# Optimization experiments

Hardware: AMD Instinct MI355X
Metric: run time of the kernel (lower is better)

## Reference

```python
import jax, jax.numpy as jnp
import numpy as np

N_NODES = 20000
D = 256            # input_dim (forced by 32x16 reshape: 2*D == 512)
N_EDGES = 320000


def _init(key, shape, scale=0.02):
    return scale * jax.random.normal(key, shape, jnp.float32)


def setup_inputs() -> dict:
    key = jax.random.key(0)
    ks = jax.random.split(key, 20)
    x = jax.random.normal(ks[0], (N_NODES, D), jnp.float32)
    edge = jax.random.randint(ks[1], (N_EDGES, 2), 0, N_NODES, dtype=jnp.int64)
    params = dict(
        W_gcn=_init(ks[2], (D, 2 * D)), b_gcn=jnp.zeros((2 * D,), jnp.float32),
        conv1_w=_init(ks[3], (1, 1, 3, 3)), conv1_b=jnp.zeros((1,), jnp.float32),
        conv2_w=_init(ks[4], (1, 1, 3, 3)), conv2_b=jnp.zeros((1,), jnp.float32),
        Wc1=_init(ks[5], (2 * D, 2 * D)), bc1=jnp.zeros((2 * D,), jnp.float32),
        Wc2=_init(ks[6], (2 * D, 2 * D)), bc2=jnp.zeros((2 * D,), jnp.float32),
        Wc3=_init(ks[7], (2 * D, 2 * D)), bc3=jnp.zeros((2 * D,), jnp.float32),
        Wp1=_init(ks[8], (4 * D, 2 * D)), bp1=jnp.zeros((2 * D,), jnp.float32),
        Wp2=_init(ks[9], (2 * D, D)), bp2=jnp.zeros((D,), jnp.float32),
        Wp3=_init(ks[10], (D, D // 2)), bp3=jnp.zeros((D // 2,), jnp.float32),
        Wp4=_init(ks[11], (D // 2, 2)), bp4=jnp.zeros((2,), jnp.float32),
    )
    return dict(x=x, edge=edge, **params)


def _gcn_conv(x, edge, W, b):
    # PyG GCNConv: add self-loops, symmetric deg^-1/2 normalization, scatter-add at dst
    src, dst = edge[:, 0], edge[:, 1]
    loops = jnp.arange(N_NODES, dtype=edge.dtype)
    src = jnp.concatenate([src, loops])
    dst = jnp.concatenate([dst, loops])
    xw = x @ W                                              # [N, 2D]
    deg = jax.ops.segment_sum(jnp.ones_like(dst, jnp.float32), dst, N_NODES)
    dinv = jnp.where(deg > 0, jax.lax.rsqrt(jnp.maximum(deg, 1e-12)), 0.0)
    norm = dinv[src] * dinv[dst]                            # [E+N]
    agg = jax.ops.segment_sum(norm[:, None] * xw[src], dst, N_NODES)
    return agg + b


def reference(x, edge, W_gcn, b_gcn, conv1_w, conv1_b, conv2_w, conv2_b,
              Wc1, bc1, Wc2, bc2, Wc3, bc3,
              Wp1, bp1, Wp2, bp2, Wp3, bp3, Wp4, bp4):
    # First stage: GCNConv + ReLU, then sum readout over nodes -> [1, 2D]
    h = jax.nn.relu(_gcn_conv(x, edge, W_gcn, b_gcn))
    h = jnp.sum(h, axis=0, keepdims=True)                   # [1, 512]

    img = h.reshape(1, 1, 32, 16)
    dn = ('NCHW', 'OIHW', 'NCHW')
    c = jax.nn.relu(jax.lax.conv_general_dilated(img, conv1_w, (1, 1), 'SAME', dimension_numbers=dn) + conv1_b.reshape(1, -1, 1, 1))
    c = jax.nn.relu(jax.lax.conv_general_dilated(c, conv2_w, (1, 1), 'SAME', dimension_numbers=dn) + conv2_b.reshape(1, -1, 1, 1))
    high_conf = jax.nn.softmax(c.reshape(1, -1), axis=1)    # [1, 512]

    # Second stage, branch B: 3-layer MLP with softmax
    f = jax.nn.relu(h @ Wc1 + bc1)
    f = jax.nn.relu(f @ Wc2 + bc2)
    front = jax.nn.softmax(f @ Wc3 + bc3, axis=1)           # [1, 512]

    complete = jnp.concatenate([high_conf, front], axis=1)  # [1, 1024]

    # Predictor MLP: 1024 -> 512 -> 256 -> 128 -> 2, sigmoid
    p = jax.nn.relu(complete @ Wp1 + bp1)
    p = jax.nn.relu(p @ Wp2 + bp2)
    p = jax.nn.relu(p @ Wp3 + bp3)
    pre = jax.nn.sigmoid(p @ Wp4 + bp4)                     # [1, 2]
    return pre
```

## Files before the change

### kernel.cpp

```cpp
#include <hip/hip_runtime.h>

#define N_NODES 20000
#define N_EDGES 320000
#define DD      256
#define D2      512
#define BCAP    64

typedef short short8 __attribute__((ext_vector_type(8)));
typedef float f32x4  __attribute__((ext_vector_type(4)));
typedef float f32x2  __attribute__((ext_vector_type(2)));

__device__ __forceinline__ unsigned f2b(float f) {
    unsigned u = __float_as_uint(f);
    u = u + 0x7fffu + ((u >> 16) & 1u);
    return u >> 16;
}

__device__ __forceinline__ unsigned f2e4m3(float f) {
    unsigned u = __float_as_uint(f);
    unsigned sg = (u >> 24) & 0x80u;
    float af = fabsf(f);
    if (af > 448.f) return sg | 0x7Eu;
    if (af < 0.015625f) {
        int i = (int)rintf(af * 512.f);
        return sg | (unsigned)i;
    }
    unsigned au = u & 0x7fffffffu;
    au += 0x7ffffu + ((au >> 20) & 1u);
    unsigned b = (au >> 20) - 960u;
    if (b > 0x7Eu) b = 0x7Eu;
    return sg | b;
}

__global__ void k1_prep(const int* __restrict__ edge, int* __restrict__ cnt,
                        int* __restrict__ csr, const float* __restrict__ x,
                        const float* __restrict__ Wg, unsigned short* __restrict__ WT,
                        unsigned* __restrict__ xf8) {
    int blk = blockIdx.x, tid = threadIdx.x;
    if (blk < 1250) {
        int e = blk * 256 + tid;
        if (e < N_EDGES) {
            int s = edge[2 * e], d = edge[2 * e + 1];
            int pos = atomicAdd(&cnt[d], 1);
            if (pos < BCAP) csr[d * BCAP + pos] = s;
        }
    } else if (blk < 1282) {
        int i = (blk - 1250) * 256 + tid;
        #pragma unroll
        for (int r = 0; r < 16; r++) {
            int idx = i + r * 8192;
            int k = idx >> 9, n = idx & 511;
            WT[n * 256 + k] = (unsigned short)f2b(Wg[idx]);
        }
    } else {
        int i = (blk - 1282) * 256 + tid;
        float4 v = ((const float4*)x)[i];
        xf8[i] = f2e4m3(v.x) | (f2e4m3(v.y) << 8) | (f2e4m3(v.z) << 16) | (f2e4m3(v.w) << 24);
    }
}

__device__ __forceinline__ float dinv_of(const int* cnt, int n) {
    return rsqrtf((float)(cnt[n] + 1));
}
__device__ __forceinline__ void acc8(float* a, float w, uint2 u) {
    f32x2 p;
    p = __builtin_amdgcn_cvt_pk_f32_fp8(u.x, false); a[0] += w * p.x; a[1] += w * p.y;
    p = __builtin_amdgcn_cvt_pk_f32_fp8(u.x, true);  a[2] += w * p.x; a[3] += w * p.y;
    p = __builtin_amdgcn_cvt_pk_f32_fp8(u.y, false); a[4] += w * p.x; a[5] += w * p.y;
    p = __builtin_amdgcn_cvt_pk_f32_fp8(u.y, true);  a[6] += w * p.x; a[7] += w * p.y;
}

__global__ void k4_agg(const int* __restrict__ cnt, const int* __restrict__ csr,
                       const unsigned char* __restrict__ xf8,
                       unsigned short* __restrict__ aggX) {
    int wid = threadIdx.x >> 6, lane = threadIdx.x & 63;
    int half = lane >> 5, l32 = lane & 31;
    int n = blockIdx.x * 4 + wid;
    float a[8] = {0.f, 0.f, 0.f, 0.f, 0.f, 0.f, 0.f, 0.f};
    if (n < N_NODES) {
        int deg = cnt[n];
        if (deg > BCAP) deg = BCAP;
        const int* bkt = csr + n * BCAP;
        int e = 0;
        for (; e + 8 <= deg; e += 8) {
            int s0 = bkt[e + 0 + half];
            int s1 = bkt[e + 2 + half];
            int s2 = bkt[e + 4 + half];
            int s3 = bkt[e + 6 + half];
            uint2 u0 = *(const uint2*)(xf8 + (size_t)s0 * DD + l32 * 8);
            uint2 u1 = *(const uint2*)(xf8 + (size_t)s1 * DD + l32 * 8);
            uint2 u2 = *(const uint2*)(xf8 + (size_t)s2 * DD + l32 * 8);
            uint2 u3 = *(const uint2*)(xf8 + (size_t)s3 * DD + l32 * 8);
            float w0 = dinv_of(cnt, s0), w1 = dinv_of(cnt, s1);
            float w2 = dinv_of(cnt, s2), w3 = dinv_of(cnt, s3);
            acc8(a, w0, u0); acc8(a, w1, u1); acc8(a, w2, u2); acc8(a, w3, u3);
        }
        for (; e + 2 <= deg; e += 2) {
            int s = bkt[e + half];
            uint2 u = *(const uint2*)(xf8 + (size_t)s * DD + l32 * 8);
            acc8(a, dinv_of(cnt, s), u);
        }
        if (e < deg && half == 0) {
            int s = bkt[e];
            uint2 u = *(const uint2*)(xf8 + (size_t)s * DD + l32 * 8);
            acc8(a, dinv_of(cnt, s), u);
        }
        #pragma unroll
        for (int j = 0; j < 8; j++) a[j] += __shfl_xor(a[j], 32, 64);
        float dn = dinv_of(cnt, n);
        float dn2 = dn * dn;
        uint2 u = *(const uint2*)(xf8 + (size_t)n * DD + l32 * 8);
        f32x2 p;
        p = __builtin_amdgcn_cvt_pk_f32_fp8(u.x, false); a[0] = dn * a[0] + dn2 * p.x; a[1] = dn * a[1] + dn2 * p.y;
        p = __builtin_amdgcn_cvt_pk_f32_fp8(u.x, true);  a[2] = dn * a[2] + dn2 * p.x; a[3] = dn * a[3] + dn2 * p.y;
        p = __builtin_amdgcn_cvt_pk_f32_fp8(u.y, false); a[4] = dn * a[4] + dn2 * p.x; a[5] = dn * a[5] + dn2 * p.y;
        p = __builtin_amdgcn_cvt_pk_f32_fp8(u.y, true);  a[6] = dn * a[6] + dn2 * p.x; a[7] = dn * a[7] + dn2 * p.y;
    }
    if (half == 0) {
        uint4 o;
        o.x = f2b(a[0]) | (f2b(a[1]) << 16);
        o.y = f2b(a[2]) | (f2b(a[3]) << 16);
        o.z = f2b(a[4]) | (f2b(a[5]) << 16);
        o.w = f2b(a[6]) | (f2b(a[7]) << 16);
        *(uint4*)(aggX + (size_t)n * DD + l32 * 8) = o;
    }
}

#define TN 128
__global__ void __launch_bounds__(256, 2)
k5_gemm(const unsigned short* __restrict__ aggX, const unsigned short* __restrict__ WT,
        const float* __restrict__ bg, float* __restrict__ h) {
    __shared__ unsigned short bsh[TN * 264];
    __shared__ float hblk[TN];
    int tid = threadIdx.x;
    int rowblk = blockIdx.x;
    int ct = blockIdx.y;
    #pragma unroll
    for (int i = 0; i < 16; i++) {
        int c = tid + i * 256;
        int r = c >> 5;
        int kc = (c & 31) << 3;
        *(short8*)(&bsh[r * 264 + kc]) = *(const short8*)(WT + (size_t)(ct * TN + r) * DD + kc);
    }
    if (tid < TN) hblk[tid] = 0.f;
    __syncthreads();

    int w = tid >> 6, lane = tid & 63;
    int quad = lane >> 4, l15 = lane & 15;
    int row = rowblk * 64 + w * 16 + l15;
    f32x4 acc[8];
    #pragma unroll
    for (int nt = 0; nt < 8; nt++) acc[nt] = (f32x4){0.f, 0.f, 0.f, 0.f};
    #pragma unroll
    for (int kt = 0; kt < 8; kt++) {
        short8 a = *(const short8*)(aggX + (size_t)row * DD + kt * 32 + quad * 8);
        #pragma unroll
        for (int nt = 0; nt < 8; nt++) {
            short8 b = *(const short8*)(&bsh[(nt * 16 + l15) * 264 + kt * 32 + quad * 8]);
            acc[nt] = __builtin_amdgcn_mfma_f32_16x16x32_bf16(a, b, acc[nt], 0, 0, 0);
        }
    }
    int rowbase = rowblk * 64 + w * 16 + quad * 4;
    #pragma unroll
    for (int nt = 0; nt < 8; nt++) {
        int cl = nt * 16 + l15;
        float bias = bg[ct * TN + cl];
        float s = 0.f;
        #pragma unroll
        for (int r = 0; r < 4; r++) {
            if (rowbase + r < N_NODES) {
                float v = acc[nt][r] + bias;
                s += v > 0.f ? v : 0.f;
            }
        }
        atomicAdd(&hblk[cl], s);
    }
    __syncthreads();
    if (tid < TN) atomicAdd(&h[ct * TN + tid], hblk[tid]);
}

__global__ void k_mv(const float* __restrict__ in, const float* __restrict__ bias,
                     const float* __restrict__ W, float* __restrict__ out, int N, int act) {
    int c = blockIdx.y * 256 + threadIdx.x;
    int k0 = blockIdx.x * 8;
    float s = 0.f;
    #pragma unroll
    for (int kk = 0; kk < 8; kk++) {
        int k = k0 + kk;
        float v = in[k];
        if (act) { v += bias[k]; v = v > 0.f ? v : 0.f; }
        s += v * W[(size_t)k * N + c];
    }
    atomicAdd(&out[c], s);
}

__global__ void k9_mid(const float* __restrict__ h, const float* __restrict__ w1, const float* __restrict__ b1,
                       const float* __restrict__ w2, const float* __restrict__ b2,
                       const float* __restrict__ l3raw, const float* __restrict__ bc3,
                       float* __restrict__ complete) {
    __shared__ float img[512];
    __shared__ float c1s[512];
    __shared__ float red[512];
    int t = threadIdx.x;
    img[t] = h[t];
    __syncthreads();
    int y = t >> 4, x = t & 15;
    float s = 0.f;
    #pragma unroll
    for (int dy = -1; dy <= 1; dy++)
        #pragma unroll
        for (int dx = -1; dx <= 1; dx++) {
            int yy = y + dy, xc = x + dx;
            if (yy >= 0 && yy < 32 && xc >= 0 && xc < 16)
                s += w1[(dy + 1) * 3 + (dx + 1)] * img[yy * 16 + xc];
        }
    s += b1[0];
    c1s[t] = s > 0.f ? s : 0.f;
    __syncthreads();
    float s2 = 0.f;
    #pragma unroll
    for (int dy = -1; dy <= 1; dy++)
        #pragma unroll
        for (int dx = -1; dx <= 1; dx++) {
            int yy = y + dy, xc = x + dx;
            if (yy >= 0 && yy < 32 && xc >= 0 && xc < 16)
                s2 += w2[(dy + 1) * 3 + (dx + 1)] * c1s[yy * 16 + xc];
        }
    s2 += b2[0];
    float v2 = s2 > 0.f ? s2 : 0.f;
    red[t] = v2; __syncthreads();
    for (int off = 256; off > 0; off >>= 1) { if (t < off) red[t] = fmaxf(red[t], red[t + off]); __syncthreads(); }
    float m = red[0]; __syncthreads();
    float e = expf(v2 - m);
    red[t] = e; __syncthreads();
    for (int off = 256; off > 0; off >>= 1) { if (t < off) red[t] += red[t + off]; __syncthreads(); }
    complete[t] = e / red[0];
    __syncthreads();
    float z = l3raw[t] + bc3[t];
    red[t] = z; __syncthreads();
    for (int off = 256; off > 0; off >>= 1) { if (t < off) red[t] = fmaxf(red[t], red[t + off]); __syncthreads(); }
    float m2 = red[0]; __syncthreads();
    float e2 = expf(z - m2);
    red[t] = e2; __syncthreads();
    for (int off = 256; off > 0; off >>= 1) { if (t < off) red[t] += red[t + off]; __syncthreads(); }
    complete[512 + t] = e2 / red[0];
}

__global__ void k12_final(const float* __restrict__ p2raw, const float* __restrict__ bp2,
                          const float* __restrict__ Wp3, const float* __restrict__ bp3,
                          const float* __restrict__ Wp4, const float* __restrict__ bp4,
                          float* __restrict__ out) {
    __shared__ float p2s[256];
    __shared__ float p3s[128];
    int t = threadIdx.x;
    float v = p2raw[t] + bp2[t];
    p2s[t] = v > 0.f ? v : 0.f;
    __syncthreads();
    if (t < 128) {
        float s = bp3[t];
        #pragma unroll 8
        for (int k = 0; k < 256; k++) s += p2s[k] * Wp3[k * 128 + t];
        p3s[t] = s > 0.f ? s : 0.f;
    }
    __syncthreads();
    if (t < 2) {
        float s = bp4[t];
        for (int k = 0; k < 128; k++) s += p3s[k] * Wp4[k * 2 + t];
        out[t] = 1.f / (1.f + expf(-s));
    }
}

extern "C" void kernel_launch(void* const* d_in, const int* in_sizes, int n_in,
                              void* d_out, int out_size, void* d_ws, size_t ws_size,
                              hipStream_t stream) {
    const float* x    = (const float*)d_in[0];
    const int*   edge = (const int*)d_in[1];
    const float* Wg   = (const float*)d_in[2];
    const float* bg   = (const float*)d_in[3];
    const float* c1w  = (const float*)d_in[4];
    const float* c1b  = (const float*)d_in[5];
    const float* c2w  = (const float*)d_in[6];
    const float* c2b  = (const float*)d_in[7];
    const float* Wc1  = (const float*)d_in[8];
    const float* bc1  = (const float*)d_in[9];
    const float* Wc2  = (const float*)d_in[10];
    const float* bc2  = (const float*)d_in[11];
    const float* Wc3  = (const float*)d_in[12];
    const float* bc3  = (const float*)d_in[13];
    const float* Wp1  = (const float*)d_in[14];
    const float* bp1  = (const float*)d_in[15];
    const float* Wp2  = (const float*)d_in[16];
    const float* bp2  = (const float*)d_in[17];
    const float* Wp3  = (const float*)d_in[18];
    const float* bp3  = (const float*)d_in[19];
    const float* Wp4  = (const float*)d_in[20];
    const float* bp4  = (const float*)d_in[21];
    float* out = (float*)d_out;

    char* ws = (char*)d_ws;
    int*   cnt      = (int*)(ws + 0);
    float* h        = (float*)(ws + 80000);
    float* f1raw    = (float*)(ws + 82048);
    float* f2raw    = (float*)(ws + 84096);
    float* l3raw    = (float*)(ws + 86144);
    float* p1raw    = (float*)(ws + 88192);
    float* p2raw    = (float*)(ws + 90240);
    float* complete = (float*)(ws + 91264);
    int*   csr      = (int*)(ws + 95360);
    unsigned short* WT   = (unsigned short*)(ws + 5215360);
    unsigned char*  xf8  = (unsigned char*)(ws + 5477504);
    unsigned short* aggX = (unsigned short*)(ws + 10597504);
    (void)ws_size; (void)in_sizes; (void)n_in; (void)out_size;

    hipMemsetAsync(d_ws, 0, 91264, stream);

    k1_prep<<<6282, 256, 0, stream>>>(edge, cnt, csr, x, Wg, WT, (unsigned*)xf8);
    k4_agg<<<5008, 256, 0, stream>>>(cnt, csr, xf8, aggX);
    k5_gemm<<<dim3(313, 4), 256, 0, stream>>>(aggX, WT, bg, h);
    k_mv<<<dim3(64, 2), 256, 0, stream>>>(h,     nullptr, Wc1, f1raw, 512, 0);
    k_mv<<<dim3(64, 2), 256, 0, stream>>>(f1raw, bc1,     Wc2, f2raw, 512, 1);
    k_mv<<<dim3(64, 2), 256, 0, stream>>>(f2raw, bc2,     Wc3, l3raw, 512, 1);
    k9_mid<<<1, 512, 0, stream>>>(h, c1w, c1b, c2w, c2b, l3raw, bc3, complete);
    k_mv<<<dim3(128, 2), 256, 0, stream>>>(complete, nullptr, Wp1, p1raw, 512, 0);
    k_mv<<<dim3(64, 1), 256, 0, stream>>>(p1raw, bp1, Wp2, p2raw, 256, 1);
    k12_final<<<1, 256, 0, stream>>>(p2raw, bp2, Wp3, bp3, Wp4, bp4, out);
}
```

Before: 214.5 us.

## Fuse tail MLP kernels via last-block pattern, deepen aggregation unroll, reduce atomics

Merges the single-block conv/softmax kernel into the preceding matrix-vector kernel and the final predictor kernel into its matrix-vector kernel, using a done counter so the last block to finish runs the tail. This removes two kernel launches and their gaps. The aggregation loop is unrolled to 16 edges so more gathers are in flight, and the GEMM epilogue reduces across quads with shuffles before the shared-memory atomic. The tradeoffs are extra fences and counter atomics, the tail now running in a single 256-thread block, and higher register pressure in the aggregation loop.

```diff
diff --git a/kernel.cpp b/kernel.cpp
--- a/kernel.cpp
+++ b/kernel.cpp
@@ -30,6 +30,10 @@
     unsigned b = (au >> 20) - 960u;
     if (b > 0x7Eu) b = 0x7Eu;
     return sg | b;
+}
+
+__device__ __forceinline__ float aload(const float* p) {
+    return __hip_atomic_load(p, __ATOMIC_RELAXED, __HIP_MEMORY_SCOPE_AGENT);
 }
 
 __global__ void k1_prep(const int* __restrict__ edge, int* __restrict__ cnt,
@@ -82,18 +86,33 @@
         if (deg > BCAP) deg = BCAP;
         const int* bkt = csr + n * BCAP;
         int e = 0;
-        for (; e + 8 <= deg; e += 8) {
-            int s0 = bkt[e + 0 + half];
-            int s1 = bkt[e + 2 + half];
-            int s2 = bkt[e + 4 + half];
-            int s3 = bkt[e + 6 + half];
+        for (; e + 16 <= deg; e += 16) {
+            int s0 = bkt[e + 0 + half],  s1 = bkt[e + 2 + half];
+            int s2 = bkt[e + 4 + half],  s3 = bkt[e + 6 + half];
+            int s4 = bkt[e + 8 + half],  s5 = bkt[e + 10 + half];
+            int s6 = bkt[e + 12 + half], s7 = bkt[e + 14 + half];
             uint2 u0 = *(const uint2*)(xf8 + (size_t)s0 * DD + l32 * 8);
             uint2 u1 = *(const uint2*)(xf8 + (size_t)s1 * DD + l32 * 8);
             uint2 u2 = *(const uint2*)(xf8 + (size_t)s2 * DD + l32 * 8);
             uint2 u3 = *(const uint2*)(xf8 + (size_t)s3 * DD + l32 * 8);
-            float w0 = dinv_of(cnt, s0), w1 = dinv_of(cnt, s1);
-            float w2 = dinv_of(cnt, s2), w3 = dinv_of(cnt, s3);
-            acc8(a, w0, u0); acc8(a, w1, u1); acc8(a, w2, u2); acc8(a, w3, u3);
+            uint2 u4 = *(const uint2*)(xf8 + (size_t)s4 * DD + l32 * 8);
+            uint2 u5 = *(const uint2*)(xf8 + (size_t)s5 * DD + l32 * 8);
+            uint2 u6 = *(const uint2*)(xf8 + (size_t)s6 * DD + l32 * 8);
+            uint2 u7 = *(const uint2*)(xf8 + (size_t)s7 * DD + l32 * 8);
+            acc8(a, dinv_of(cnt, s0), u0); acc8(a, dinv_of(cnt, s1), u1);
+            acc8(a, dinv_of(cnt, s2), u2); acc8(a, dinv_of(cnt, s3), u3);
+            acc8(a, dinv_of(cnt, s4), u4); acc8(a, dinv_of(cnt, s5), u5);
+            acc8(a, dinv_of(cnt, s6), u6); acc8(a, dinv_of(cnt, s7), u7);
+        }
+        for (; e + 8 <= deg; e += 8) {
+            int s0 = bkt[e + 0 + half], s1 = bkt[e + 2 + half];
+            int s2 = bkt[e + 4 + half], s3 = bkt[e + 6 + half];
+            uint2 u0 = *(const uint2*)(xf8 + (size_t)s0 * DD + l32 * 8);
+            uint2 u1 = *(const uint2*)(xf8 + (size_t)s1 * DD + l32 * 8);
+            uint2 u2 = *(const uint2*)(xf8 + (size_t)s2 * DD + l32 * 8);
+            uint2 u3 = *(const uint2*)(xf8 + (size_t)s3 * DD + l32 * 8);
+            acc8(a, dinv_of(cnt, s0), u0); acc8(a, dinv_of(cnt, s1), u1);
+            acc8(a, dinv_of(cnt, s2), u2); acc8(a, dinv_of(cnt, s3), u3);
         }
         for (; e + 2 <= deg; e += 2) {
             int s = bkt[e + half];
@@ -173,7 +192,9 @@
                 s += v > 0.f ? v : 0.f;
             }
         }
-        atomicAdd(&hblk[cl], s);
+        s += __shfl_xor(s, 16, 64);
+        s += __shfl_xor(s, 32, 64);
+        if (quad == 0) atomicAdd(&hblk[cl], s);
     }
     __syncthreads();
     if (tid < TN) atomicAdd(&h[ct * TN + tid], hblk[tid]);
@@ -194,79 +215,136 @@
     atomicAdd(&out[c], s);
 }
 
-__global__ void k9_mid(const float* __restrict__ h, const float* __restrict__ w1, const float* __restrict__ b1,
-                       const float* __restrict__ w2, const float* __restrict__ b2,
-                       const float* __restrict__ l3raw, const float* __restrict__ bc3,
-                       float* __restrict__ complete) {
+__global__ void k_mv_k9(const float* __restrict__ in, const float* __restrict__ bias,
+                        const float* __restrict__ W, float* __restrict__ l3raw,
+                        const float* __restrict__ h,
+                        const float* __restrict__ c1w, const float* __restrict__ c1b,
+                        const float* __restrict__ c2w, const float* __restrict__ c2b,
+                        const float* __restrict__ bc3,
+                        float* __restrict__ complete, int* __restrict__ done) {
     __shared__ float img[512];
     __shared__ float c1s[512];
-    __shared__ float red[512];
-    int t = threadIdx.x;
-    img[t] = h[t];
-    __syncthreads();
-    int y = t >> 4, x = t & 15;
-    float s = 0.f;
-    #pragma unroll
-    for (int dy = -1; dy <= 1; dy++)
-        #pragma unroll
-        for (int dx = -1; dx <= 1; dx++) {
-            int yy = y + dy, xc = x + dx;
-            if (yy >= 0 && yy < 32 && xc >= 0 && xc < 16)
-                s += w1[(dy + 1) * 3 + (dx + 1)] * img[yy * 16 + xc];
-        }
-    s += b1[0];
-    c1s[t] = s > 0.f ? s : 0.f;
-    __syncthreads();
-    float s2 = 0.f;
-    #pragma unroll
-    for (int dy = -1; dy <= 1; dy++)
-        #pragma unroll
-        for (int dx = -1; dx <= 1; dx++) {
-            int yy = y + dy, xc = x + dx;
-            if (yy >= 0 && yy < 32 && xc >= 0 && xc < 16)
-                s2 += w2[(dy + 1) * 3 + (dx + 1)] * c1s[yy * 16 + xc];
-        }
-    s2 += b2[0];
-    float v2 = s2 > 0.f ? s2 : 0.f;
-    red[t] = v2; __syncthreads();
-    for (int off = 256; off > 0; off >>= 1) { if (t < off) red[t] = fmaxf(red[t], red[t + off]); __syncthreads(); }
+    __shared__ float red[256];
+    __shared__ int lastflag;
+    int tid = threadIdx.x;
+    {
+        int c = blockIdx.y * 256 + tid;
+        int k0 = blockIdx.x * 8;
+        float s = 0.f;
+        #pragma unroll
+        for (int kk = 0; kk < 8; kk++) {
+            int k = k0 + kk;
+            float v = in[k] + bias[k];
+            v = v > 0.f ? v : 0.f;
+            s += v * W[k * 512 + c];
+        }
+        atomicAdd(&l3raw[c], s);
+    }
+    __threadfence();
+    if (tid == 0) lastflag = (atomicAdd(done, 1) == 127);
+    __syncthreads();
+    if (!lastflag) return;
+    __threadfence();
+    img[tid] = h[tid]; img[tid + 256] = h[tid + 256];
+    __syncthreads();
+    float cv[2];
+    #pragma unroll
+    for (int p = 0; p < 2; p++) {
+        int pix = tid + p * 256;
+        int y = pix >> 4, x = pix & 15;
+        float s = 0.f;
+        #pragma unroll
+        for (int dy = -1; dy <= 1; dy++)
+            #pragma unroll
+            for (int dx = -1; dx <= 1; dx++) {
+                int yy = y + dy, xc = x + dx;
+                if (yy >= 0 && yy < 32 && xc >= 0 && xc < 16)
+                    s += c1w[(dy + 1) * 3 + (dx + 1)] * img[yy * 16 + xc];
+            }
+        s += c1b[0];
+        cv[p] = s > 0.f ? s : 0.f;
+    }
+    c1s[tid] = cv[0]; c1s[tid + 256] = cv[1];
+    __syncthreads();
+    float v2[2];
+    #pragma unroll
+    for (int p = 0; p < 2; p++) {
+        int pix = tid + p * 256;
+        int y = pix >> 4, x = pix & 15;
+        float s = 0.f;
+        #pragma unroll
+        for (int dy = -1; dy <= 1; dy++)
+            #pragma unroll
+            for (int dx = -1; dx <= 1; dx++) {
+                int yy = y + dy, xc = x + dx;
+                if (yy >= 0 && yy < 32 && xc >= 0 && xc < 16)
+                    s += c2w[(dy + 1) * 3 + (dx + 1)] * c1s[yy * 16 + xc];
+            }
+        s += c2b[0];
+        v2[p] = s > 0.f ? s : 0.f;
+    }
+    red[tid] = fmaxf(v2[0], v2[1]); __syncthreads();
+    for (int off = 128; off > 0; off >>= 1) { if (tid < off) red[tid] = fmaxf(red[tid], red[tid + off]); __syncthreads(); }
     float m = red[0]; __syncthreads();
-    float e = expf(v2 - m);
-    red[t] = e; __syncthreads();
-    for (int off = 256; off > 0; off >>= 1) { if (t < off) red[t] += red[t + off]; __syncthreads(); }
-    complete[t] = e / red[0];
-    __syncthreads();
-    float z = l3raw[t] + bc3[t];
-    red[t] = z; __syncthreads();
-    for (int off = 256; off > 0; off >>= 1) { if (t < off) red[t] = fmaxf(red[t], red[t + off]); __syncthreads(); }
+    float e0 = expf(v2[0] - m), e1 = expf(v2[1] - m);
+    red[tid] = e0 + e1; __syncthreads();
+    for (int off = 128; off > 0; off >>= 1) { if (tid < off) red[tid] += red[tid + off]; __syncthreads(); }
+    float inv = 1.f / red[0];
+    complete[tid] = e0 * inv; complete[tid + 256] = e1 * inv;
+    __syncthreads();
+    float z0 = aload(&l3raw[tid]) + bc3[tid];
+    float z1 = aload(&l3raw[tid + 256]) + bc3[tid + 256];
+    red[tid] = fmaxf(z0, z1); __syncthreads();
+    for (int off = 128; off > 0; off >>= 1) { if (tid < off) red[tid] = fmaxf(red[tid], red[tid + off]); __syncthreads(); }
     float m2 = red[0]; __syncthreads();
-    float e2 = expf(z - m2);
-    red[t] = e2; __syncthreads();
-    for (int off = 256; off > 0; off >>= 1) { if (t < off) red[t] += red[t + off]; __syncthreads(); }
-    complete[512 + t] = e2 / red[0];
-}
-
-__global__ void k12_final(const float* __restrict__ p2raw, const float* __restrict__ bp2,
-                          const float* __restrict__ Wp3, const float* __restrict__ bp3,
-                          const float* __restrict__ Wp4, const float* __restrict__ bp4,
-                          float* __restrict__ out) {
+    float g0 = expf(z0 - m2), g1 = expf(z1 - m2);
+    red[tid] = g0 + g1; __syncthreads();
+    for (int off = 128; off > 0; off >>= 1) { if (tid < off) red[tid] += red[tid + off]; __syncthreads(); }
+    float inv2 = 1.f / red[0];
+    complete[512 + tid] = g0 * inv2; complete[768 + tid] = g1 * inv2;
+}
+
+__global__ void k_mv_k12(const float* __restrict__ in, const float* __restrict__ bias,
+                         const float* __restrict__ W, float* __restrict__ p2raw,
+                         const float* __restrict__ bp2,
+                         const float* __restrict__ Wp3, const float* __restrict__ bp3,
+                         const float* __restrict__ Wp4, const float* __restrict__ bp4,
+                         float* __restrict__ out, int* __restrict__ done) {
     __shared__ float p2s[256];
     __shared__ float p3s[128];
-    int t = threadIdx.x;
-    float v = p2raw[t] + bp2[t];
-    p2s[t] = v > 0.f ? v : 0.f;
-    __syncthreads();
-    if (t < 128) {
-        float s = bp3[t];
+    __shared__ int lastflag;
+    int tid = threadIdx.x;
+    {
+        int k0 = blockIdx.x * 8;
+        float s = 0.f;
+        #pragma unroll
+        for (int kk = 0; kk < 8; kk++) {
+            int k = k0 + kk;
+            float v = in[k] + bias[k];
+            v = v > 0.f ? v : 0.f;
+            s += v * W[k * 256 + tid];
+        }
+        atomicAdd(&p2raw[tid], s);
+    }
+    __threadfence();
+    if (tid == 0) lastflag = (atomicAdd(done, 1) == 63);
+    __syncthreads();
+    if (!lastflag) return;
+    __threadfence();
+    float v = aload(&p2raw[tid]) + bp2[tid];
+    p2s[tid] = v > 0.f ? v : 0.f;
+    __syncthreads();
+    if (tid < 128) {
+        float s = bp3[tid];
         #pragma unroll 8
-        for (int k = 0; k < 256; k++) s += p2s[k] * Wp3[k * 128 + t];
-        p3s[t] = s > 0.f ? s : 0.f;
-    }
-    __syncthreads();
-    if (t < 2) {
-        float s = bp4[t];
-        for (int k = 0; k < 128; k++) s += p3s[k] * Wp4[k * 2 + t];
-        out[t] = 1.f / (1.f + expf(-s));
+        for (int k = 0; k < 256; k++) s += p2s[k] * Wp3[k * 128 + tid];
+        p3s[tid] = s > 0.f ? s : 0.f;
+    }
+    __syncthreads();
+    if (tid < 2) {
+        float s = bp4[tid];
+        for (int k = 0; k < 128; k++) s += p3s[k] * Wp4[k * 2 + tid];
+        out[tid] = 1.f / (1.f + expf(-s));
     }
 }
 
@@ -305,23 +383,25 @@
     float* l3raw    = (float*)(ws + 86144);
     float* p1raw    = (float*)(ws + 88192);
     float* p2raw    = (float*)(ws + 90240);
-    float* complete = (float*)(ws + 91264);
-    int*   csr      = (int*)(ws + 95360);
-    unsigned short* WT   = (unsigned short*)(ws + 5215360);
-    unsigned char*  xf8  = (unsigned char*)(ws + 5477504);
-    unsigned short* aggX = (unsigned short*)(ws + 10597504);
+    int*   done9    = (int*)(ws + 91264);
+    int*   done12   = (int*)(ws + 91268);
+    float* complete = (float*)(ws + 91280);
+    int*   csr      = (int*)(ws + 95376);
+    unsigned short* WT   = (unsigned short*)(ws + 5215376);
+    unsigned char*  xf8  = (unsigned char*)(ws + 5477520);
+    unsigned short* aggX = (unsigned short*)(ws + 10597520);
     (void)ws_size; (void)in_sizes; (void)n_in; (void)out_size;
 
-    hipMemsetAsync(d_ws, 0, 91264, stream);
+    hipMemsetAsync(d_ws, 0, 91272, stream);
 
     k1_prep<<<6282, 256, 0, stream>>>(edge, cnt, csr, x, Wg, WT, (unsigned*)xf8);
     k4_agg<<<5008, 256, 0, stream>>>(cnt, csr, xf8, aggX);
     k5_gemm<<<dim3(313, 4), 256, 0, stream>>>(aggX, WT, bg, h);
     k_mv<<<dim3(64, 2), 256, 0, stream>>>(h,     nullptr, Wc1, f1raw, 512, 0);
     k_mv<<<dim3(64, 2), 256, 0, stream>>>(f1raw, bc1,     Wc2, f2raw, 512, 1);
-    k_mv<<<dim3(64, 2), 256, 0, stream>>>(f2raw, bc2,     Wc3, l3raw, 512, 1);
-    k9_mid<<<1, 512, 0, stream>>>(h, c1w, c1b, c2w, c2b, l3raw, bc3, complete);
+    k_mv_k9<<<dim3(64, 2), 256, 0, stream>>>(f2raw, bc2, Wc3, l3raw, h,
+                                             c1w, c1b, c2w, c2b, bc3, complete, done9);
     k_mv<<<dim3(128, 2), 256, 0, stream>>>(complete, nullptr, Wp1, p1raw, 512, 0);
-    k_mv<<<dim3(64, 1), 256, 0, stream>>>(p1raw, bp1, Wp2, p2raw, 256, 1);
-    k12_final<<<1, 256, 0, stream>>>(p2raw, bp2, Wp3, bp3, Wp4, bp4, out);
-}
+    k_mv_k12<<<64, 256, 0, stream>>>(p1raw, bp1, Wp2, p2raw, bp2,
+                                     Wp3, bp3, Wp4, bp4, out, done12);
+}
```

Result: slower. 222.1 us (+3.5%).
